# Performance work log

Measured on AMD Instinct MI355X. Metric: run time of the kernel, lower is better.

The kernel has to match this reference:

```python
import jax, jax.numpy as jnp
import numpy as np

N = 131072          # source points
M = 65536           # sampled (query) points
NN = 32             # max_nr_neighbors
K = 15              # num_kernel_points
IN_F = 64
OUT_F = 128
MAP_SIZE = 40.0
SUB_DIST = 0.5      # subsampling_dist * subsampling_factor (meters)
KERNEL_RADIUS = max(1.5, 2.0 * SUB_DIST) / MAP_SIZE          # 0.0375
KP_EXTENT = KERNEL_RADIUS / (K ** (1.0 / 3.0) - 1.0) * 1.5
NEG_SLOPE = 0.01    # nn.LeakyReLU default


def setup_inputs() -> dict:
    rng = np.random.RandomState(0)
    points = rng.rand(N, 3).astype(np.float32)

    # ---- gridSampling (faithful numpy port of the torch code) ----
    resolution = SUB_DIST / MAP_SIZE
    grid = np.floor(points / resolution)
    center = (grid + 0.5) * resolution
    dist = ((points - center) ** 2).sum(1)
    dist = dist / dist.max() * 0.7
    v_size = np.ceil(1.0 / resolution)
    grid_idx = grid[:, 0] + grid[:, 1] * v_size + grid[:, 2] * v_size * v_size
    grid_d = grid_idx + dist
    order = np.argsort(grid_d, kind='stable')
    gi_sorted = grid_idx[order]
    first = np.ones(N, bool)
    first[1:] = gi_sorted[1:] != gi_sorted[:-1]
    sample_idx = order[first]  # closest-to-voxel-center point per voxel
    if sample_idx.shape[0] < M:
        sample_idx = np.tile(sample_idx, int(np.ceil(M / sample_idx.shape[0])))
    sample_idx = np.sort(sample_idx[:M])

    # ---- radius search (stand-in for octree.radiusSearchIndices) ----
    # candidates = window in voxel-sorted order, filtered by true euclidean radius,
    # nearest-first, padded with shadow index N (standard KPConv padding).
    pos_in_sorted = np.empty(N, np.int64)
    pos_in_sorted[order] = np.arange(N)
    qpos = pos_in_sorted[sample_idx]
    offs = np.arange(-48, 48)
    cand_pos = np.clip(qpos[:, None] + offs[None, :], 0, N - 1)
    cand_idx = order[cand_pos]                                  # [M,96]
    d2 = ((points[cand_idx] - points[sample_idx][:, None, :]) ** 2).sum(-1)
    valid = d2 <= KERNEL_RADIUS ** 2
    d2w = np.where(valid, d2, np.inf)
    sel = np.argsort(d2w, axis=1)[:, :NN]
    nbr = np.take_along_axis(cand_idx, sel, 1)
    nbr_ok = np.take_along_axis(valid, sel, 1)
    neighbors_index = np.where(nbr_ok, nbr, N).astype(np.int32)  # [M,NN]

    # ---- kernel point dispositions (rigid KPConv buffer) ----
    kp_dir = rng.randn(K, 3).astype(np.float32)
    kp_dir /= np.linalg.norm(kp_dir, axis=1, keepdims=True) + 1e-9
    kernel_points = kp_dir * (rng.rand(K, 1).astype(np.float32) ** (1.0 / 3.0)) * KERNEL_RADIUS

    key = jax.random.key(0)
    ks = jax.random.split(key, 6)
    def lin(k, i, o):
        return (jax.random.normal(k, (i, o), jnp.float32) / np.sqrt(i)).astype(jnp.float32)

    return {
        'points': jnp.asarray(points),
        'features': jax.random.normal(ks[0], (N, IN_F), jnp.float32),
        'W_pre': lin(ks[1], IN_F, OUT_F),
        'b_pre': jnp.zeros((OUT_F,), jnp.float32),
        'kernel_points': jnp.asarray(kernel_points),
        'kp_weights': jax.random.normal(ks[2], (K, OUT_F, OUT_F), jnp.float32) / np.sqrt(K * OUT_F),
        'W_post': lin(ks[3], OUT_F, OUT_F),
        'b_post': jnp.zeros((OUT_F,), jnp.float32),
        'W_sc': lin(ks[4], IN_F, OUT_F),
        'b_sc': jnp.zeros((OUT_F,), jnp.float32),
        'sample_idx': jnp.asarray(sample_idx, jnp.int32),
        'neighbors_index': jnp.asarray(neighbors_index),
    }


def _leaky(x):
    return jnp.where(x >= 0, x, NEG_SLOPE * x)


def reference(points, features, W_pre, b_pre, kernel_points, kp_weights,
              W_post, b_post, W_sc, b_sc, sample_idx, neighbors_index):
    # preactivation: Linear + LeakyReLU (batchnorm=False)
    feats = _leaky(features @ W_pre + b_pre)                       # [N, OUT_F]

    # shadow padding: far point + zero feature row at index N
    s_pts = jnp.concatenate([points, jnp.full((1, 3), 1e6, points.dtype)], 0)
    x_pad = jnp.concatenate([feats, jnp.zeros((1, OUT_F), feats.dtype)], 0)

    # rigid KPConv: gather -> distance influence -> weight -> aggregate
    q_pts = points[sample_idx]                                     # [M,3]
    neighb = s_pts[neighbors_index] - q_pts[:, None, :]            # [M,NN,3]
    sq_d = jnp.sum((neighb[:, :, None, :] - kernel_points[None, None]) ** 2, -1)  # [M,NN,K]
    all_w = jnp.maximum(1.0 - jnp.sqrt(sq_d) / KP_EXTENT, 0.0)     # linear influence
    nx = x_pad[neighbors_index]                                    # [M,NN,OUT_F]
    wfeat = jnp.einsum('mnk,mnc->mkc', all_w, nx)                  # [M,K,OUT_F]
    conv = jnp.einsum('mkc,kco->mo', wfeat, kp_weights)            # [M,OUT_F]

    # post layer: LeakyReLU then Linear (batchnorm=False, relu=True)
    post = _leaky(conv) @ W_post + b_post

    # shortcut on sampled input features (in_fdim != out_fdim -> Linear)
    sc = features[sample_idx] @ W_sc + b_sc
    return _leaky(sc + post)                                       # [M,OUT_F]
```

## Files before the change

kernel.cpp:

```cpp
#include <hip/hip_runtime.h>
#include <cmath>

#define NPTS 131072
#define MTOT 65536
#define NNB  32
#define KKP  15
#define INF  64
#define OUTF 128
#define KCDIM 1920
#define ROWB 3840

typedef __attribute__((ext_vector_type(8))) __bf16 bf16x8;
typedef __attribute__((ext_vector_type(8))) unsigned short u16x8;
typedef __attribute__((ext_vector_type(4))) float f32x4;
typedef unsigned int u32;

__device__ __forceinline__ float bf2f(u32 v){ return __builtin_bit_cast(float, v<<16); }
__device__ __forceinline__ u32 f2bf(float f){
  u32 u = __builtin_bit_cast(u32, f);
  return (u + 0x7fffu + ((u>>16)&1u)) >> 16;
}
__device__ __forceinline__ float leaky(float v){ return v >= 0.f ? v : 0.01f*v; }

__device__ __forceinline__ void g2l16(const void* g, void* l){
  __builtin_amdgcn_global_load_lds((const __attribute__((address_space(1))) u32*)g,
                                   (__attribute__((address_space(3))) u32*)l, 16, 0, 0);
}

__global__ __launch_bounds__(256) void k_cvt_67723(
    const float* __restrict__ kpw, const float* __restrict__ wpost,
    const float* __restrict__ wsc, const float* __restrict__ wpre,
    unsigned short* __restrict__ kpwT, unsigned short* __restrict__ wpostT,
    unsigned short* __restrict__ wscT, unsigned short* __restrict__ wpreT)
{
  int tid = blockIdx.x * 256 + threadIdx.x;
  if (tid < OUTF * KCDIM) {
    int o = tid / KCDIM, kc = tid % KCDIM;
    kpwT[tid] = (unsigned short)f2bf(kpw[(size_t)kc * OUTF + o]);
    return;
  }
  int t2 = tid - OUTF * KCDIM;
  if (t2 < OUTF * OUTF) {
    int o = t2 / OUTF, i = t2 % OUTF;
    wpostT[t2] = (unsigned short)f2bf(wpost[i * OUTF + o]);
    return;
  }
  int t3 = t2 - OUTF * OUTF;
  if (t3 < OUTF * INF) {
    int o = t3 / INF, c = t3 % INF;
    wscT[t3] = (unsigned short)f2bf(wsc[c * OUTF + o]);
    return;
  }
  int t4 = t3 - OUTF * INF;
  if (t4 < OUTF * INF) {
    int o = t4 / INF, c = t4 % INF;
    wpreT[t4] = (unsigned short)f2bf(wpre[c * OUTF + o]);
  }
}

__global__ __launch_bounds__(256) void k_pre_67723(
    const float* __restrict__ feat, const unsigned short* __restrict__ wpreT,
    const float* __restrict__ bp, unsigned short* __restrict__ featbf)
{
  const int w = threadIdx.x >> 6, l = threadIdx.x & 63, lr = l & 15, lg = l >> 4;
  const int m0 = blockIdx.x * 128 + w * 32;
  f32x4 acc[2][8];
#pragma unroll
  for (int ot = 0; ot < 8; ot++) {
    float bv = bp[ot*16 + lr];
    f32x4 s = {bv, bv, bv, bv};
    acc[0][ot] = s; acc[1][ot] = s;
  }
  bf16x8 af[2][2];
#pragma unroll
  for (int mi = 0; mi < 2; mi++)
#pragma unroll
  for (int ks = 0; ks < 2; ks++) {
    const float* src = feat + (size_t)(m0 + mi*16 + lr) * INF + ks*32 + lg*8;
    float4 f0 = *(const float4*)src, f1 = *(const float4*)(src + 4);
    u16x8 p;
    p[0]=f2bf(f0.x); p[1]=f2bf(f0.y); p[2]=f2bf(f0.z); p[3]=f2bf(f0.w);
    p[4]=f2bf(f1.x); p[5]=f2bf(f1.y); p[6]=f2bf(f1.z); p[7]=f2bf(f1.w);
    af[mi][ks] = __builtin_bit_cast(bf16x8, p);
  }
#pragma unroll
  for (int ks = 0; ks < 2; ks++)
#pragma unroll
  for (int ot = 0; ot < 8; ot++) {
    bf16x8 b = *(const bf16x8*)(wpreT + (size_t)(ot*16 + lr) * INF + ks*32 + lg*8);
    acc[0][ot] = __builtin_amdgcn_mfma_f32_16x16x32_bf16(af[0][ks], b, acc[0][ot], 0,0,0);
    acc[1][ot] = __builtin_amdgcn_mfma_f32_16x16x32_bf16(af[1][ks], b, acc[1][ot], 0,0,0);
  }
#pragma unroll
  for (int mi = 0; mi < 2; mi++)
#pragma unroll
  for (int ot = 0; ot < 8; ot++)
#pragma unroll
  for (int r = 0; r < 4; r++) {
    int m = m0 + mi*16 + lg*4 + r;
    featbf[(size_t)m * OUTF + ot*16 + lr] = (unsigned short)f2bf(leaky(acc[mi][ot][r]));
  }
}

__global__ __launch_bounds__(256) void k_wfeat_67723(
    const float* __restrict__ points, const float* __restrict__ kp,
    const int* __restrict__ sample_idx, const int* __restrict__ nbr,
    const unsigned short* __restrict__ featbf, unsigned short* __restrict__ wfeat,
    float inv_ext, int mbase)
{
  const int w = threadIdx.x >> 6, l = threadIdx.x & 63;
  const int s2 = (blockIdx.x * 4 + w) * 2;
  const int half = l >> 5, n_ = l & 31;
  const int gm = mbase + s2 + half;
  const int sidx = sample_idx[gm];
  const float qx = points[sidx*3+0], qy = points[sidx*3+1], qz = points[sidx*3+2];
  const int ni = nbr[(size_t)gm * NNB + n_];
  const bool valid = ni < NPTS;
  const int nic = valid ? ni : 0;
  const u32 nboff = (u32)nic * (OUTF * 2);
  const float px = points[nic*3+0], py = points[nic*3+1], pz = points[nic*3+2];
  const float dx = px - qx, dy = py - qy, dz = pz - qz;
  float wk[KKP];
#pragma unroll
  for (int k = 0; k < KKP; k++) {
    float ex = dx - kp[k*3+0], ey = dy - kp[k*3+1], ez = dz - kp[k*3+2];
    float d = sqrtf(ex*ex + ey*ey + ez*ez);
    float wv = fmaxf(1.f - d * inv_ext, 0.f);
    wk[k] = valid ? wv : 0.f;
  }
  unsigned long long bal = __ballot(valid);
  const int cA = __popcll(bal & 0xffffffffull);
  const int cB = __popcll(bal >> 32);
  const char* fb = (const char*)featbf;
#pragma unroll
  for (int h2 = 0; h2 < 2; h2++) {
    const int cnt = h2 ? cB : cA;
    float a0[KKP], a1[KKP];
#pragma unroll
    for (int k = 0; k < KKP; k++) { a0[k] = 0.f; a1[k] = 0.f; }
#pragma unroll
    for (int n = 0; n < NNB; n++) {
      if (n >= cnt) break;
      u32 off = (u32)__builtin_amdgcn_readlane((int)nboff, h2*32 + n);
      u32 xu = *(const u32*)(fb + off + l*4);
      float x0 = bf2f(xu & 0xffffu), x1 = bf2f(xu >> 16);
#pragma unroll
      for (int k = 0; k < KKP; k++) {
        float wv = __builtin_bit_cast(float,
            __builtin_amdgcn_readlane(__builtin_bit_cast(int, wk[k]), h2*32 + n));
        a0[k] = fmaf(wv, x0, a0[k]);
        a1[k] = fmaf(wv, x1, a1[k]);
      }
    }
    u32* drow = (u32*)(wfeat + (size_t)(s2 + h2) * KCDIM);
#pragma unroll
    for (int k = 0; k < KKP; k++)
      drow[k*64 + l] = f2bf(a0[k]) | (f2bf(a1[k]) << 16);
  }
}

__global__ __launch_bounds__(256) void k_conv_67723(
    const unsigned short* __restrict__ wfeat, const unsigned short* __restrict__ kpwT,
    const unsigned short* __restrict__ wpostT, const unsigned short* __restrict__ wscT,
    const float* __restrict__ features, const float* __restrict__ bpost,
    const float* __restrict__ bsc, const int* __restrict__ sample_idx,
    float* __restrict__ out, int mbase)
{
  extern __shared__ char smem[];
  const int t = threadIdx.x, w = t >> 6, l = t & 63, lr = l & 15, lg = l >> 4;
  const int m0 = blockIdx.x * 128;

  f32x4 acc[2][8];
#pragma unroll
  for (int mi = 0; mi < 2; mi++)
#pragma unroll
  for (int ot = 0; ot < 8; ot++) acc[mi][ot] = (f32x4){0,0,0,0};

  const char* arows = (const char*)wfeat + (size_t)m0 * ROWB;
  const char* brows = (const char*)kpwT;
  const int qbase = w * 4;
  const int srow = l >> 3;
  const int sinner = ((l & 7) * 16) ^ (srow << 4);

#pragma unroll
  for (int j = 0; j < 4; j++) {
    int q = qbase + j; int m = q*8 + srow;
    g2l16(arows + (size_t)m * ROWB + sinner, smem + q*1024);
    g2l16(brows + (size_t)m * ROWB + sinner, smem + 16384 + q*1024);
  }
  __syncthreads();

  for (int kt = 0; kt < 30; kt++) {
    const int cur = kt & 1;
    const int nxt_off = (cur ^ 1) << 15;
    if (kt < 29) {
      const int kb = (kt + 1) * 128;
#pragma unroll
      for (int j = 0; j < 4; j++) {
        int q = qbase + j; int m = q*8 + srow;
        g2l16(arows + (size_t)m * ROWB + kb + sinner, smem + nxt_off + q*1024);
        g2l16(brows + (size_t)m * ROWB + kb + sinner, smem + nxt_off + 16384 + q*1024);
      }
    }
    const char* Ab = smem + (cur << 15);
    const char* Bb = Ab + 16384;
#pragma unroll
    for (int ks = 0; ks < 2; ks++) {
      bf16x8 af[2];
#pragma unroll
      for (int mi = 0; mi < 2; mi++) {
        int m = (w*2 + mi)*16 + lr;
        af[mi] = *(const bf16x8*)(Ab + m*128 + ((ks*64 + lg*16) ^ ((m & 7) << 4)));
      }
#pragma unroll
      for (int ot = 0; ot < 8; ot++) {
        int o = ot*16 + lr;
        bf16x8 bfr = *(const bf16x8*)(Bb + o*128 + ((ks*64 + lg*16) ^ ((o & 7) << 4)));
        acc[0][ot] = __builtin_amdgcn_mfma_f32_16x16x32_bf16(af[0], bfr, acc[0][ot], 0,0,0);
        acc[1][ot] = __builtin_amdgcn_mfma_f32_16x16x32_bf16(af[1], bfr, acc[1][ot], 0,0,0);
      }
    }
    __syncthreads();
  }

  char* a2 = smem;
  char* a3 = smem + 32768;
#pragma unroll
  for (int mi = 0; mi < 2; mi++)
#pragma unroll
  for (int ot = 0; ot < 8; ot++)
#pragma unroll
  for (int r = 0; r < 4; r++) {
    int m = (w*2 + mi)*16 + lg*4 + r;
    int o = ot*16 + lr;
    *(unsigned short*)(a2 + m*256 + ((o*2) ^ ((m & 15) << 4))) =
        (unsigned short)f2bf(leaky(acc[mi][ot][r]));
  }
  {
    int r = t >> 1, h = t & 1;
    int sidx = sample_idx[mbase + m0 + r];
    const float* src = features + (size_t)sidx * INF + h*32;
#pragma unroll
    for (int qq = 0; qq < 4; qq++) {
      float4 f0 = *(const float4*)(src + qq*8);
      float4 f1 = *(const float4*)(src + qq*8 + 4);
      uint4 pv = make_uint4(f2bf(f0.x) | (f2bf(f0.y) << 16),
                            f2bf(f0.z) | (f2bf(f0.w) << 16),
                            f2bf(f1.x) | (f2bf(f1.y) << 16),
                            f2bf(f1.z) | (f2bf(f1.w) << 16));
      *(uint4*)(a3 + r*128 + ((h*64 + qq*16) ^ ((r & 7) << 4))) = pv;
    }
  }
  __syncthreads();

  f32x4 d[2][8];
#pragma unroll
  for (int ot = 0; ot < 8; ot++) {
    float bv = bpost[ot*16 + lr] + bsc[ot*16 + lr];
    f32x4 s = {bv, bv, bv, bv};
    d[0][ot] = s; d[1][ot] = s;
  }
#pragma unroll
  for (int st = 0; st < 4; st++) {
    bf16x8 af[2];
#pragma unroll
    for (int mi = 0; mi < 2; mi++) {
      int m = (w*2 + mi)*16 + lr;
      af[mi] = *(const bf16x8*)(a2 + m*256 + ((st*64 + lg*16) ^ ((m & 15) << 4)));
    }
#pragma unroll
    for (int ot = 0; ot < 8; ot++) {
      bf16x8 b = *(const bf16x8*)(wpostT + (size_t)(ot*16 + lr) * OUTF + st*32 + lg*8);
      d[0][ot] = __builtin_amdgcn_mfma_f32_16x16x32_bf16(af[0], b, d[0][ot], 0,0,0);
      d[1][ot] = __builtin_amdgcn_mfma_f32_16x16x32_bf16(af[1], b, d[1][ot], 0,0,0);
    }
  }
#pragma unroll
  for (int st = 0; st < 2; st++) {
    bf16x8 af[2];
#pragma unroll
    for (int mi = 0; mi < 2; mi++) {
      int m = (w*2 + mi)*16 + lr;
      af[mi] = *(const bf16x8*)(a3 + m*128 + ((st*64 + lg*16) ^ ((m & 7) << 4)));
    }
#pragma unroll
    for (int ot = 0; ot < 8; ot++) {
      bf16x8 b = *(const bf16x8*)(wscT + (size_t)(ot*16 + lr) * INF + st*32 + lg*8);
      d[0][ot] = __builtin_amdgcn_mfma_f32_16x16x32_bf16(af[0], b, d[0][ot], 0,0,0);
      d[1][ot] = __builtin_amdgcn_mfma_f32_16x16x32_bf16(af[1], b, d[1][ot], 0,0,0);
    }
  }
#pragma unroll
  for (int mi = 0; mi < 2; mi++)
#pragma unroll
  for (int ot = 0; ot < 8; ot++)
#pragma unroll
  for (int r = 0; r < 4; r++) {
    int m = (w*2 + mi)*16 + lg*4 + r;
    out[(size_t)(mbase + m0 + m) * OUTF + ot*16 + lr] = leaky(d[mi][ot][r]);
  }
}

extern "C" void kernel_launch(void* const* d_in, const int* in_sizes, int n_in,
                              void* d_out, int out_size, void* d_ws, size_t ws_size,
                              hipStream_t stream)
{
  const float* points   = (const float*)d_in[0];
  const float* features = (const float*)d_in[1];
  const float* W_pre    = (const float*)d_in[2];
  const float* b_pre    = (const float*)d_in[3];
  const float* kpts     = (const float*)d_in[4];
  const float* kpw      = (const float*)d_in[5];
  const float* W_post   = (const float*)d_in[6];
  const float* b_post   = (const float*)d_in[7];
  const float* W_sc     = (const float*)d_in[8];
  const float* b_sc     = (const float*)d_in[9];
  const int* sample_idx = (const int*)d_in[10];
  const int* nbr        = (const int*)d_in[11];
  float* out = (float*)d_out;

  char* ws = (char*)d_ws;
  unsigned short* featbf = (unsigned short*)ws;
  unsigned short* kpwT   = (unsigned short*)(ws + 33554432);
  unsigned short* wpostT = (unsigned short*)(ws + 34045952);
  unsigned short* wscT   = (unsigned short*)(ws + 34078720);
  unsigned short* wpreT  = (unsigned short*)(ws + 34095104);
  unsigned short* wfeat  = (unsigned short*)(ws + 34111488);

  double ext = (1.5 / 40.0) / (pow(15.0, 1.0 / 3.0) - 1.0) * 1.5;
  float inv_ext = (float)(1.0 / ext);

  size_t fixed = 34111488ull;
  int chunks = 1;
  while (chunks < 32 && fixed + 251658240ull / (size_t)chunks > ws_size) chunks <<= 1;
  int msz = MTOT / chunks;

  (void)hipFuncSetAttribute((const void*)k_conv_67723,
                            hipFuncAttributeMaxDynamicSharedMemorySize, 65536);

  k_cvt_67723<<<1088, 256, 0, stream>>>(kpw, W_post, W_sc, W_pre, kpwT, wpostT, wscT, wpreT);
  k_pre_67723<<<1024, 256, 0, stream>>>(features, wpreT, b_pre, featbf);
  for (int ci = 0; ci < chunks; ci++) {
    k_wfeat_67723<<<msz/8, 256, 0, stream>>>(points, kpts, sample_idx, nbr, featbf,
                                             wfeat, inv_ext, ci*msz);
    k_conv_67723<<<msz/128, 256, 65536, stream>>>(wfeat, kpwT, wpostT, wscT, features,
                                                  b_post, b_sc, sample_idx, out, ci*msz);
  }
}
```

Baseline: 200.3 us.

## Compute KP-weighted neighbor aggregation with MFMA and widen conv blocks to 512 threads

The neighbor-feature aggregation kernel previously did scalar FMAs using readlane broadcasts of the per-neighbor kernel weights. It now stages neighbor offsets and addresses in shared memory and builds a bf16 weight fragment of size K by 32 neighbors. It then uses 16x16x32 bf16 MFMAs against gathered feature fragments, with a blocked workgroup swizzle. The conv kernel is also reorganized to 8 waves, splitting the output columns across wave pairs, to lower per-wave accumulator pressure. The cost is that the influence weights are now rounded to bf16 before accumulation, and invalid neighbors are still gathered from row 0 with zero weight.

```diff
diff --git a/kernel.cpp b/kernel.cpp
--- a/kernel.cpp
+++ b/kernel.cpp
@@ -102,64 +102,98 @@
   }
 }
 
-__global__ __launch_bounds__(256) void k_wfeat_67723(
+__global__ __launch_bounds__(256) void k_wfmma_67723(
     const float* __restrict__ points, const float* __restrict__ kp,
     const int* __restrict__ sample_idx, const int* __restrict__ nbr,
     const unsigned short* __restrict__ featbf, unsigned short* __restrict__ wfeat,
-    float inv_ext, int mbase)
-{
-  const int w = threadIdx.x >> 6, l = threadIdx.x & 63;
-  const int s2 = (blockIdx.x * 4 + w) * 2;
-  const int half = l >> 5, n_ = l & 31;
-  const int gm = mbase + s2 + half;
-  const int sidx = sample_idx[gm];
-  const float qx = points[sidx*3+0], qy = points[sidx*3+1], qz = points[sidx*3+2];
-  const int ni = nbr[(size_t)gm * NNB + n_];
-  const bool valid = ni < NPTS;
-  const int nic = valid ? ni : 0;
-  const u32 nboff = (u32)nic * (OUTF * 2);
-  const float px = points[nic*3+0], py = points[nic*3+1], pz = points[nic*3+2];
-  const float dx = px - qx, dy = py - qy, dz = pz - qz;
-  float wk[KKP];
-#pragma unroll
-  for (int k = 0; k < KKP; k++) {
-    float ex = dx - kp[k*3+0], ey = dy - kp[k*3+1], ez = dz - kp[k*3+2];
-    float d = sqrtf(ex*ex + ey*ey + ez*ez);
-    float wv = fmaxf(1.f - d * inv_ext, 0.f);
-    wk[k] = valid ? wv : 0.f;
-  }
-  unsigned long long bal = __ballot(valid);
-  const int cA = __popcll(bal & 0xffffffffull);
-  const int cB = __popcll(bal >> 32);
+    float inv_ext, int mbase, int nwg)
+{
+  __shared__ float4 meta[16][32];
+  const int bid = blockIdx.x;
+  const int swb = (bid & 7) * (nwg >> 3) + (bid >> 3);
+  const int m0l = swb * 16;
+  const int gm0 = mbase + m0l;
+  const int t = threadIdx.x;
+
+  for (int e = t; e < 512; e += 256) {
+    int s = e >> 5, n = e & 31;
+    int gm = gm0 + s;
+    int sidx = sample_idx[gm];
+    int ni = nbr[(size_t)gm * NNB + n];
+    bool valid = ni < NPTS;
+    int nic = valid ? ni : 0;
+    float qx = points[sidx*3], qy = points[sidx*3+1], qz = points[sidx*3+2];
+    float dx = points[nic*3] - qx, dy = points[nic*3+1] - qy, dz = points[nic*3+2] - qz;
+    if (!valid) dx = 1e9f;
+    meta[s][n] = make_float4(dx, dy, dz, __int_as_float(nic * (OUTF*2)));
+  }
+  __syncthreads();
+
+  const int l = t & 63, w = t >> 6, lr = l & 15, lg = l >> 4;
+  const bool kvalid = lr < KKP;
+  const int kk = kvalid ? lr : 0;
+  const float kx = kp[kk*3], ky = kp[kk*3+1], kz = kp[kk*3+2];
   const char* fb = (const char*)featbf;
-#pragma unroll
-  for (int h2 = 0; h2 < 2; h2++) {
-    const int cnt = h2 ? cB : cA;
-    float a0[KKP], a1[KKP];
-#pragma unroll
-    for (int k = 0; k < KKP; k++) { a0[k] = 0.f; a1[k] = 0.f; }
-#pragma unroll
-    for (int n = 0; n < NNB; n++) {
-      if (n >= cnt) break;
-      u32 off = (u32)__builtin_amdgcn_readlane((int)nboff, h2*32 + n);
-      u32 xu = *(const u32*)(fb + off + l*4);
-      float x0 = bf2f(xu & 0xffffu), x1 = bf2f(xu >> 16);
-#pragma unroll
-      for (int k = 0; k < KKP; k++) {
-        float wv = __builtin_bit_cast(float,
-            __builtin_amdgcn_readlane(__builtin_bit_cast(int, wk[k]), h2*32 + n));
-        a0[k] = fmaf(wv, x0, a0[k]);
-        a1[k] = fmaf(wv, x1, a1[k]);
-      }
-    }
-    u32* drow = (u32*)(wfeat + (size_t)(s2 + h2) * KCDIM);
-#pragma unroll
-    for (int k = 0; k < KKP; k++)
-      drow[k*64 + l] = f2bf(a0[k]) | (f2bf(a1[k]) << 16);
-  }
-}
-
-__global__ __launch_bounds__(256) void k_conv_67723(
+  const f32x4 zero = {0,0,0,0};
+
+  for (int i = 0; i < 4; i++) {
+    const int s = w*4 + i;
+    float4 mj[8];
+#pragma unroll
+    for (int j = 0; j < 8; j++) mj[j] = meta[s][lg*8 + j];
+
+    u32 apk[4];
+#pragma unroll
+    for (int j2 = 0; j2 < 4; j2++) {
+      u32 lohi[2];
+#pragma unroll
+      for (int h = 0; h < 2; h++) {
+        float4 m_ = mj[2*j2 + h];
+        float ex = m_.x - kx, ey = m_.y - ky, ez = m_.z - kz;
+        float d = sqrtf(ex*ex + ey*ey + ez*ez);
+        float wv = fmaxf(1.f - d * inv_ext, 0.f);
+        lohi[h] = kvalid ? f2bf(wv) : 0u;
+      }
+      apk[j2] = lohi[0] | (lohi[1] << 16);
+    }
+    bf16x8 afr = __builtin_bit_cast(bf16x8, apk);
+
+#pragma unroll
+    for (int t2 = 0; t2 < 2; t2++) {
+      uint2 dj[8];
+#pragma unroll
+      for (int j = 0; j < 8; j++) {
+        u32 off = __builtin_bit_cast(u32, mj[j].w);
+        dj[j] = *(const uint2*)(fb + off + t2*128 + lr*8);
+      }
+      f32x4 D[4];
+#pragma unroll
+      for (int q = 0; q < 4; q++) {
+        u32 b[4];
+#pragma unroll
+        for (int u = 0; u < 4; u++) {
+          u32 w0 = (q < 2) ? dj[2*u].x   : dj[2*u].y;
+          u32 w1 = (q < 2) ? dj[2*u+1].x : dj[2*u+1].y;
+          b[u] = __builtin_amdgcn_perm(w1, w0, (q & 1) ? 0x07060302u : 0x05040100u);
+        }
+        D[q] = __builtin_amdgcn_mfma_f32_16x16x32_bf16(
+                   afr, __builtin_bit_cast(bf16x8, b), zero, 0,0,0);
+      }
+#pragma unroll
+      for (int r = 0; r < 4; r++) {
+        int kr = lg*4 + r;
+        if (kr < KKP) {
+          uint2 pv;
+          pv.x = f2bf(D[0][r]) | (f2bf(D[1][r]) << 16);
+          pv.y = f2bf(D[2][r]) | (f2bf(D[3][r]) << 16);
+          *(uint2*)((char*)wfeat + (size_t)(m0l + s) * ROWB + kr*256 + t2*128 + lr*8) = pv;
+        }
+      }
+    }
+  }
+}
+
+__global__ __launch_bounds__(512) void k_conv_67723(
     const unsigned short* __restrict__ wfeat, const unsigned short* __restrict__ kpwT,
     const unsigned short* __restrict__ wpostT, const unsigned short* __restrict__ wscT,
     const float* __restrict__ features, const float* __restrict__ bpost,
@@ -168,25 +202,24 @@
 {
   extern __shared__ char smem[];
   const int t = threadIdx.x, w = t >> 6, l = t & 63, lr = l & 15, lg = l >> 4;
+  const int mq = w >> 1, oh = w & 1;
   const int m0 = blockIdx.x * 128;
 
-  f32x4 acc[2][8];
-#pragma unroll
-  for (int mi = 0; mi < 2; mi++)
-#pragma unroll
-  for (int ot = 0; ot < 8; ot++) acc[mi][ot] = (f32x4){0,0,0,0};
+  f32x4 acc[2][4];
+#pragma unroll
+  for (int mi = 0; mi < 2; mi++)
+#pragma unroll
+  for (int ot = 0; ot < 4; ot++) acc[mi][ot] = (f32x4){0,0,0,0};
 
   const char* arows = (const char*)wfeat + (size_t)m0 * ROWB;
   const char* brows = (const char*)kpwT;
-  const int qbase = w * 4;
-  const int srow = l >> 3;
-  const int sinner = ((l & 7) * 16) ^ (srow << 4);
-
-#pragma unroll
-  for (int j = 0; j < 4; j++) {
-    int q = qbase + j; int m = q*8 + srow;
-    g2l16(arows + (size_t)m * ROWB + sinner, smem + q*1024);
-    g2l16(brows + (size_t)m * ROWB + sinner, smem + 16384 + q*1024);
+
+#pragma unroll
+  for (int h = 0; h < 2; h++) {
+    int c = t + h*512; int row = c >> 3; int col = c & 7;
+    int sinner = (col*16) ^ ((row & 7) << 4);
+    g2l16(arows + (size_t)row * ROWB + sinner, smem + c*16);
+    g2l16(brows + (size_t)row * ROWB + sinner, smem + 16384 + c*16);
   }
   __syncthreads();
 
@@ -196,10 +229,11 @@
     if (kt < 29) {
       const int kb = (kt + 1) * 128;
 #pragma unroll
-      for (int j = 0; j < 4; j++) {
-        int q = qbase + j; int m = q*8 + srow;
-        g2l16(arows + (size_t)m * ROWB + kb + sinner, smem + nxt_off + q*1024);
-        g2l16(brows + (size_t)m * ROWB + kb + sinner, smem + nxt_off + 16384 + q*1024);
+      for (int h = 0; h < 2; h++) {
+        int c = t + h*512; int row = c >> 3; int col = c & 7;
+        int sinner = (col*16) ^ ((row & 7) << 4);
+        g2l16(arows + (size_t)row * ROWB + kb + sinner, smem + nxt_off + c*16);
+        g2l16(brows + (size_t)row * ROWB + kb + sinner, smem + nxt_off + 16384 + c*16);
       }
     }
     const char* Ab = smem + (cur << 15);
@@ -209,12 +243,12 @@
       bf16x8 af[2];
 #pragma unroll
       for (int mi = 0; mi < 2; mi++) {
-        int m = (w*2 + mi)*16 + lr;
+        int m = mq*32 + mi*16 + lr;
         af[mi] = *(const bf16x8*)(Ab + m*128 + ((ks*64 + lg*16) ^ ((m & 7) << 4)));
       }
 #pragma unroll
-      for (int ot = 0; ot < 8; ot++) {
-        int o = ot*16 + lr;
+      for (int ot = 0; ot < 4; ot++) {
+        int o = oh*64 + ot*16 + lr;
         bf16x8 bfr = *(const bf16x8*)(Bb + o*128 + ((ks*64 + lg*16) ^ ((o & 7) << 4)));
         acc[0][ot] = __builtin_amdgcn_mfma_f32_16x16x32_bf16(af[0], bfr, acc[0][ot], 0,0,0);
         acc[1][ot] = __builtin_amdgcn_mfma_f32_16x16x32_bf16(af[1], bfr, acc[1][ot], 0,0,0);
@@ -228,64 +262,60 @@
 #pragma unroll
   for (int mi = 0; mi < 2; mi++)
 #pragma unroll
-  for (int ot = 0; ot < 8; ot++)
+  for (int ot = 0; ot < 4; ot++)
 #pragma unroll
   for (int r = 0; r < 4; r++) {
-    int m = (w*2 + mi)*16 + lg*4 + r;
-    int o = ot*16 + lr;
+    int m = mq*32 + mi*16 + lg*4 + r;
+    int o = oh*64 + ot*16 + lr;
     *(unsigned short*)(a2 + m*256 + ((o*2) ^ ((m & 15) << 4))) =
         (unsigned short)f2bf(leaky(acc[mi][ot][r]));
   }
-  {
-    int r = t >> 1, h = t & 1;
+  for (int e = t; e < 1024; e += 512) {
+    int r = e >> 3, seg = e & 7;
     int sidx = sample_idx[mbase + m0 + r];
-    const float* src = features + (size_t)sidx * INF + h*32;
-#pragma unroll
-    for (int qq = 0; qq < 4; qq++) {
-      float4 f0 = *(const float4*)(src + qq*8);
-      float4 f1 = *(const float4*)(src + qq*8 + 4);
-      uint4 pv = make_uint4(f2bf(f0.x) | (f2bf(f0.y) << 16),
-                            f2bf(f0.z) | (f2bf(f0.w) << 16),
-                            f2bf(f1.x) | (f2bf(f1.y) << 16),
-                            f2bf(f1.z) | (f2bf(f1.w) << 16));
-      *(uint4*)(a3 + r*128 + ((h*64 + qq*16) ^ ((r & 7) << 4))) = pv;
-    }
+    const float* src = features + (size_t)sidx * INF + seg*8;
+    float4 f0 = *(const float4*)src, f1 = *(const float4*)(src + 4);
+    uint4 pv = make_uint4(f2bf(f0.x) | (f2bf(f0.y) << 16),
+                          f2bf(f0.z) | (f2bf(f0.w) << 16),
+                          f2bf(f1.x) | (f2bf(f1.y) << 16),
+                          f2bf(f1.z) | (f2bf(f1.w) << 16));
+    *(uint4*)(a3 + r*128 + ((seg*16) ^ ((r & 7) << 4))) = pv;
   }
   __syncthreads();
 
-  f32x4 d[2][8];
-#pragma unroll
-  for (int ot = 0; ot < 8; ot++) {
-    float bv = bpost[ot*16 + lr] + bsc[ot*16 + lr];
+  f32x4 d[2][4];
+#pragma unroll
+  for (int ot = 0; ot < 4; ot++) {
+    float bv = bpost[oh*64 + ot*16 + lr] + bsc[oh*64 + ot*16 + lr];
     f32x4 s = {bv, bv, bv, bv};
     d[0][ot] = s; d[1][ot] = s;
   }
 #pragma unroll
-  for (int st = 0; st < 4; st++) {
+  for (int ks = 0; ks < 4; ks++) {
     bf16x8 af[2];
 #pragma unroll
     for (int mi = 0; mi < 2; mi++) {
-      int m = (w*2 + mi)*16 + lr;
-      af[mi] = *(const bf16x8*)(a2 + m*256 + ((st*64 + lg*16) ^ ((m & 15) << 4)));
-    }
-#pragma unroll
-    for (int ot = 0; ot < 8; ot++) {
-      bf16x8 b = *(const bf16x8*)(wpostT + (size_t)(ot*16 + lr) * OUTF + st*32 + lg*8);
+      int m = mq*32 + mi*16 + lr;
+      af[mi] = *(const bf16x8*)(a2 + m*256 + ((ks*64 + lg*16) ^ ((m & 15) << 4)));
+    }
+#pragma unroll
+    for (int ot = 0; ot < 4; ot++) {
+      bf16x8 b = *(const bf16x8*)(wpostT + (size_t)(oh*64 + ot*16 + lr) * OUTF + ks*32 + lg*8);
       d[0][ot] = __builtin_amdgcn_mfma_f32_16x16x32_bf16(af[0], b, d[0][ot], 0,0,0);
       d[1][ot] = __builtin_amdgcn_mfma_f32_16x16x32_bf16(af[1], b, d[1][ot], 0,0,0);
     }
   }
 #pragma unroll
-  for (int st = 0; st < 2; st++) {
+  for (int ks = 0; ks < 2; ks++) {
     bf16x8 af[2];
 #pragma unroll
     for (int mi = 0; mi < 2; mi++) {
-      int m = (w*2 + mi)*16 + lr;
-      af[mi] = *(const bf16x8*)(a3 + m*128 + ((st*64 + lg*16) ^ ((m & 7) << 4)));
-    }
-#pragma unroll
-    for (int ot = 0; ot < 8; ot++) {
-      bf16x8 b = *(const bf16x8*)(wscT + (size_t)(ot*16 + lr) * INF + st*32 + lg*8);
+      int m = mq*32 + mi*16 + lr;
+      af[mi] = *(const bf16x8*)(a3 + m*128 + ((ks*64 + lg*16) ^ ((m & 7) << 4)));
+    }
+#pragma unroll
+    for (int ot = 0; ot < 4; ot++) {
+      bf16x8 b = *(const bf16x8*)(wscT + (size_t)(oh*64 + ot*16 + lr) * INF + ks*32 + lg*8);
       d[0][ot] = __builtin_amdgcn_mfma_f32_16x16x32_bf16(af[0], b, d[0][ot], 0,0,0);
       d[1][ot] = __builtin_amdgcn_mfma_f32_16x16x32_bf16(af[1], b, d[1][ot], 0,0,0);
     }
@@ -293,11 +323,12 @@
 #pragma unroll
   for (int mi = 0; mi < 2; mi++)
 #pragma unroll
-  for (int ot = 0; ot < 8; ot++)
+  for (int ot = 0; ot < 4; ot++)
 #pragma unroll
   for (int r = 0; r < 4; r++) {
-    int m = (w*2 + mi)*16 + lg*4 + r;
-    out[(size_t)(mbase + m0 + m) * OUTF + ot*16 + lr] = leaky(d[mi][ot][r]);
+    int m = mq*32 + mi*16 + lg*4 + r;
+    int o = oh*64 + ot*16 + lr;
+    out[(size_t)(mbase + m0 + m) * OUTF + o] = leaky(d[mi][ot][r]);
   }
 }
 
@@ -341,9 +372,10 @@
   k_cvt_67723<<<1088, 256, 0, stream>>>(kpw, W_post, W_sc, W_pre, kpwT, wpostT, wscT, wpreT);
   k_pre_67723<<<1024, 256, 0, stream>>>(features, wpreT, b_pre, featbf);
   for (int ci = 0; ci < chunks; ci++) {
-    k_wfeat_67723<<<msz/8, 256, 0, stream>>>(points, kpts, sample_idx, nbr, featbf,
-                                             wfeat, inv_ext, ci*msz);
-    k_conv_67723<<<msz/128, 256, 65536, stream>>>(wfeat, kpwT, wpostT, wscT, features,
+    int nwg = msz / 16;
+    k_wfmma_67723<<<nwg, 256, 0, stream>>>(points, kpts, sample_idx, nbr, featbf,
+                                           wfeat, inv_ext, ci*msz, nwg);
+    k_conv_67723<<<msz/128, 512, 65536, stream>>>(wfeat, kpwT, wpostT, wscT, features,
                                                   b_post, b_sc, sample_idx, out, ci*msz);
   }
 }
```

New measurement: 167.5 us. 16.4% less time.
